# Optimization experiments

Hardware: AMD Instinct MI355X
Metric: run time of the kernel (lower is better)

The kernel has to match this reference:

```python
import jax, jax.numpy as jnp
import numpy as np

B, H, W = 8, 512, 512
KSIZE = 11   # HVS Gaussian kernel size
SIGMA = 2.0
EPS = 1e-8


def _gauss_kernel():
    ax = jnp.arange(KSIZE, dtype=jnp.float32) - (KSIZE - 1) / 2.0
    g = jnp.exp(-(ax ** 2) / (2.0 * SIGMA ** 2))
    k = jnp.outer(g, g)
    return k / jnp.sum(k)


def _conv_same(x, k):
    # x: (B,1,H,W), k: (kh,kw) symmetric -> conv == correlation
    return jax.lax.conv_general_dilated(
        x, k[None, None, :, :], window_strides=(1, 1), padding='SAME',
        dimension_numbers=('NCHW', 'OIHW', 'NCHW'))


def setup_inputs() -> dict:
    key = jax.random.key(0)
    k1, k2, k3 = jax.random.split(key, 3)
    prob_map = jax.random.uniform(k1, (B, 1, H, W), dtype=jnp.float32,
                                  minval=0.01, maxval=0.99)
    c = jax.random.uniform(k2, (B, 1, H, W), dtype=jnp.float32)
    # binary halftone sampled per-pixel from prob_map
    h_sampled = (jax.random.uniform(k3, (B, 1, H, W)) < prob_map).astype(jnp.float32)
    return {"prob_map": prob_map, "c": c, "h_sampled": h_sampled}


def reference(prob_map, c, h_sampled):
    k = _gauss_kernel()
    # perceived error of the sampled halftone: e = G*h - c
    e = _conv_same(h_sampled, k) - c                     # (B,1,H,W)
    corr = _conv_same(e, k)                              # (G*e), G symmetric
    sum_k2 = jnp.sum(k * k)
    delta = 1.0 - 2.0 * h_sampled                        # flip change per pixel
    # reward_calc.compute_reward_with_flip, vectorized over all pixels:
    # E(flip at a) - E = 2*delta_a*(G*e)(a) + delta_a^2 * sum(G^2)
    reward = 2.0 * delta * corr + (delta ** 2) * sum_k2  # >0 means flip hurts
    log_prob = jnp.where(h_sampled > 0.5,
                         jnp.log(prob_map + EPS),
                         jnp.log(1.0 - prob_map + EPS))
    # local expected-gradient (REINFORCE) loss, averaged over batch
    loss = -jnp.sum(reward * log_prob) / prob_map.shape[0]
    return loss
```

## Files before the change

### kernel.cpp

```cpp
#include <hip/hip_runtime.h>

typedef float v2f __attribute__((ext_vector_type(2)));
typedef float v4f __attribute__((ext_vector_type(4)));

#define IMG 512
#define TS  32
#define NBLK 2048

#define A_STR  58
#define BT_STR 46
#define ET_STR 44
#define CT_STR 36

__device__ __forceinline__ v2f lo2(v4f v) { return __builtin_shufflevector(v, v, 0, 1); }
__device__ __forceinline__ v2f hi2(v4f v) { return __builtin_shufflevector(v, v, 2, 3); }

__device__ __forceinline__ v4f ldq(const float* __restrict__ hmap, size_t base,
                                   int x0, int y0, int idx) {
    int r = idx / 14, q = idx - r * 14;
    int gy = y0 - 10 + r, gx0 = x0 - 12 + 4 * q;
    v4f v = {0.f, 0.f, 0.f, 0.f};
    if ((unsigned)gy < IMG) {
        const float* hr = &hmap[base + ((size_t)gy << 9)];
        if (gx0 >= 0 && gx0 + 3 < IMG) {
            v = *(const v4f*)&hr[gx0];
        } else {
            if ((unsigned)(gx0 + 0) < IMG) v.x = hr[gx0 + 0];
            if ((unsigned)(gx0 + 1) < IMG) v.y = hr[gx0 + 1];
            if ((unsigned)(gx0 + 2) < IMG) v.z = hr[gx0 + 2];
            if ((unsigned)(gx0 + 3) < IMG) v.w = hr[gx0 + 3];
        }
    }
    return v;
}

__global__ __launch_bounds__(256, 6) void marl_fused(
    const float* __restrict__ prob,
    const float* __restrict__ cmap,
    const float* __restrict__ hmap,
    float* __restrict__ out)
{
    __shared__ __align__(16) float Abuf[52 * A_STR];
    __shared__ __align__(16) float Bbuf[56 * BT_STR];
    __shared__ float red[4];

    const float W[11] = {0.00881223f, 0.02714358f, 0.06511405f, 0.12164908f,
                         0.17699840f, 0.20056540f, 0.17699840f, 0.12164908f,
                         0.06511405f, 0.02714358f, 0.00881223f};
    v2f wv[11];
#pragma unroll
    for (int i = 0; i < 11; ++i) wv[i] = (v2f){W[i], W[i]};
    float w2 = 0.f;
#pragma unroll
    for (int i = 0; i < 11; ++i) w2 += W[i] * W[i];
    const float sumk2 = w2 * w2;
    const v2f z = {0.f, 0.f};

    const int tid = threadIdx.x;
    const int i0 = tid, i1 = tid + 256, i2 = tid + 512;

    const int T  = blockIdx.x;
    const int b  = T >> 8, r8 = T & 255;
    const int x0 = (r8 & 15) * TS, y0 = (r8 >> 4) * TS;
    const size_t base = (size_t)b << 18;

    const int p1run = tid % 7, p1q = tid / 7;
    const int p2p = tid % 21, p2eq = tid / 21;
    const int p3oyq = tid & 3, p3ex = tid >> 2;
    const int oy0e = 2 * (tid & 15), ox0 = 2 * (tid >> 4);

    v2f hv[2], pv[2];
    float creg[2][4];
    {
        v4f ha = ldq(hmap, base, x0, y0, i0);
        v4f hb = ldq(hmap, base, x0, y0, i1);
        v4f hc = (tid < 216) ? ldq(hmap, base, x0, y0, i2) : (v4f){0.f,0.f,0.f,0.f};
        if (tid < 231) {
#pragma unroll
            for (int h = 0; h < 2; ++h) {
                int gy = y0 - 5 + 2 * p2p + h;
#pragma unroll
                for (int c = 0; c < 4; ++c) {
                    int gx = x0 - 5 + 4 * p2eq + c;
                    creg[h][c] = ((unsigned)gy < IMG && (unsigned)gx < IMG)
                        ? cmap[base + ((size_t)gy << 9) + gx] : 0.f;
                }
            }
        }
#pragma unroll
        for (int h = 0; h < 2; ++h) {
            size_t rowb = base + ((size_t)(y0 + oy0e + h) << 9) + (x0 + ox0);
            hv[h] = *(const v2f*)&hmap[rowb];
            pv[h] = *(const v2f*)&prob[rowb];
        }
        { int r = i0 / 14, q = i0 - r * 14; *(v4f*)&Abuf[r * A_STR + 4 * q] = ha; }
        { int r = i1 / 14, q = i1 - r * 14; *(v4f*)&Abuf[r * A_STR + 4 * q] = hb; }
        if (tid < 216) { int r = i2 / 14, q = i2 - r * 14; *(v4f*)&Abuf[r * A_STR + 4 * q] = hc; }
    }
    __syncthreads();

    if (tid < 98) {
        int by0 = 6 * p1run;
        v2f accLo[6] = {z, z, z, z, z, z}, accHi[6] = {z, z, z, z, z, z};
#pragma unroll
        for (int i = 0; i < 16; ++i) {
            v4f a = *(const v4f*)&Abuf[(by0 + i) * A_STR + 4 * p1q];
            v2f lo = lo2(a), hi = hi2(a);
#pragma unroll
            for (int r = 0; r < 6; ++r) {
                int j = i - r;
                if (j >= 0 && j < 11) { accLo[r] += wv[j] * lo; accHi[r] += wv[j] * hi; }
            }
        }
#pragma unroll
        for (int r = 0; r < 6; ++r) {
            int by = by0 + r;
            Bbuf[(4 * p1q + 0) * BT_STR + by] = accLo[r].x;
            Bbuf[(4 * p1q + 1) * BT_STR + by] = accLo[r].y;
            Bbuf[(4 * p1q + 2) * BT_STR + by] = accHi[r].x;
            Bbuf[(4 * p1q + 3) * BT_STR + by] = accHi[r].y;
        }
    }
    __syncthreads();

    if (tid < 231) {
        int ex0 = 4 * p2eq, ey0 = 2 * p2p;
        v2f acc[4] = {z, z, z, z};
#pragma unroll
        for (int i = 0; i < 14; ++i) {
            v2f bb = *(const v2f*)&Bbuf[(ex0 + 2 + i) * BT_STR + ey0];
#pragma unroll
            for (int c = 0; c < 4; ++c) {
                int j = i - c;
                if (j >= 0 && j < 11) acc[c] += wv[j] * bb;
            }
        }
#pragma unroll
        for (int c = 0; c < 4; ++c) {
            int ex = ex0 + c;
            if (ex < 42) {
                int gx = x0 - 5 + ex;
                bool xin = (unsigned)gx < IMG;
#pragma unroll
                for (int h = 0; h < 2; ++h) {
                    int gy = y0 - 5 + ey0 + h;
                    float v = 0.f;
                    if (xin && (unsigned)gy < IMG)
                        v = acc[c][h] - creg[h][c];
                    Abuf[ex * ET_STR + ey0 + h] = v;
                }
            }
        }
    }
    __syncthreads();

    if (tid < 168) {
        int oy0 = 8 * p3oyq;
        const float* src = &Abuf[p3ex * ET_STR + oy0];
        v4f w0 = *(const v4f*)&src[0];
        v4f w1 = *(const v4f*)&src[4];
        v4f w2_ = *(const v4f*)&src[8];
        v4f w3 = *(const v4f*)&src[12];
        v4f w4 = *(const v4f*)&src[16];
        float win[20];
        *(v4f*)&win[0] = w0; *(v4f*)&win[4] = w1; *(v4f*)&win[8] = w2_;
        *(v4f*)&win[12] = w3; *(v4f*)&win[16] = w4;
        float o[8];
#pragma unroll
        for (int k = 0; k < 8; ++k) {
            float acc = 0.f;
#pragma unroll
            for (int j = 0; j < 11; ++j) acc += W[j] * win[k + j];
            o[k] = acc;
        }
        *(v4f*)&Bbuf[p3ex * CT_STR + oy0]     = (v4f){o[0], o[1], o[2], o[3]};
        *(v4f*)&Bbuf[p3ex * CT_STR + oy0 + 4] = (v4f){o[4], o[5], o[6], o[7]};
    }
    __syncthreads();

    float partial = 0.f;
    {
        v2f acc[2] = {z, z};
#pragma unroll
        for (int i = 0; i < 12; ++i) {
            v2f ct = *(const v2f*)&Bbuf[(ox0 + i) * CT_STR + oy0e];
#pragma unroll
            for (int c = 0; c < 2; ++c) {
                int j = i - c;
                if (j >= 0 && j < 11) acc[c] += wv[j] * ct;
            }
        }
#pragma unroll
        for (int h = 0; h < 2; ++h) {
#pragma unroll
            for (int c = 0; c < 2; ++c) {
                float h_ = hv[h][c], p_ = pv[h][c];
                float logp = __logf(h_ > 0.5f ? p_ + 1e-8f : 1.f - p_ + 1e-8f);
                float delta = 1.f - 2.f * h_;
                partial += (2.f * delta * acc[c][h] + sumk2) * logp;
            }
        }
    }

#pragma unroll
    for (int off = 32; off > 0; off >>= 1)
        partial += __shfl_down(partial, off, 64);
    if ((tid & 63) == 0) red[tid >> 6] = partial;
    __syncthreads();
    if (tid == 0) {
        float s = red[0] + red[1] + red[2] + red[3];
        atomicAdd(out, s * -0.125f);
    }
}

extern "C" void kernel_launch(void* const* d_in, const int* in_sizes, int n_in,
                              void* d_out, int out_size, void* d_ws, size_t ws_size,
                              hipStream_t stream) {
    const float* prob = (const float*)d_in[0];
    const float* cmap = (const float*)d_in[1];
    const float* hmap = (const float*)d_in[2];
    float* out = (float*)d_out;

    hipMemsetAsync(out, 0, sizeof(float), stream);

    marl_fused<<<dim3(NBLK), dim3(256), 0, stream>>>(prob, cmap, hmap, out);
}
```

Before: 103.1 us.

## Widen tiles to 64x32 and replace atomic accumulation with a two-pass reduction

Output tiles grow from 32x32 to 64x32 pixels, which halves the block count and cuts the relative overhead of the 10-pixel halo on both separable convolution passes. Each thread in every stage now handles more outputs. The memset and per-block atomicAdd are replaced by per-block partial sums written to the workspace and reduced by a second single-block kernel, which also makes the sum deterministic. In exchange, shared memory per block and register pressure rise, occupancy drops to 4 blocks per SIMD, and the extra kernel launch adds some fixed latency.

```diff
diff --git a/kernel.cpp b/kernel.cpp
--- a/kernel.cpp
+++ b/kernel.cpp
@@ -4,10 +4,9 @@
 typedef float v4f __attribute__((ext_vector_type(4)));
 
 #define IMG 512
-#define TS  32
-#define NBLK 2048
-
-#define A_STR  58
+#define NBLK 1024
+
+#define A_STR  92
 #define BT_STR 46
 #define ET_STR 44
 #define CT_STR 36
@@ -17,7 +16,7 @@
 
 __device__ __forceinline__ v4f ldq(const float* __restrict__ hmap, size_t base,
                                    int x0, int y0, int idx) {
-    int r = idx / 14, q = idx - r * 14;
+    int r = idx / 22, q = idx - r * 22;
     int gy = y0 - 10 + r, gx0 = x0 - 12 + 4 * q;
     v4f v = {0.f, 0.f, 0.f, 0.f};
     if ((unsigned)gy < IMG) {
@@ -34,14 +33,14 @@
     return v;
 }
 
-__global__ __launch_bounds__(256, 6) void marl_fused(
+__global__ __launch_bounds__(256, 4) void marl_fused(
     const float* __restrict__ prob,
     const float* __restrict__ cmap,
     const float* __restrict__ hmap,
-    float* __restrict__ out)
+    float* __restrict__ ws)
 {
     __shared__ __align__(16) float Abuf[52 * A_STR];
-    __shared__ __align__(16) float Bbuf[56 * BT_STR];
+    __shared__ __align__(16) float Bbuf[88 * BT_STR];
     __shared__ float red[4];
 
     const float W[11] = {0.00881223f, 0.02714358f, 0.06511405f, 0.12164908f,
@@ -57,31 +56,31 @@
     const v2f z = {0.f, 0.f};
 
     const int tid = threadIdx.x;
-    const int i0 = tid, i1 = tid + 256, i2 = tid + 512;
-
     const int T  = blockIdx.x;
-    const int b  = T >> 8, r8 = T & 255;
-    const int x0 = (r8 & 15) * TS, y0 = (r8 >> 4) * TS;
+    const int b  = T >> 7, r7 = T & 127;
+    const int x0 = (r7 & 7) << 6, y0 = (r7 >> 3) << 5;
     const size_t base = (size_t)b << 18;
 
     const int p1run = tid % 7, p1q = tid / 7;
-    const int p2p = tid % 21, p2eq = tid / 21;
-    const int p3oyq = tid & 3, p3ex = tid >> 2;
-    const int oy0e = 2 * (tid & 15), ox0 = 2 * (tid >> 4);
-
-    v2f hv[2], pv[2];
-    float creg[2][4];
+    const int p2p = tid % 21, p2exo = tid / 21;
+    const int p3ex = tid >> 1, p3oy0 = (tid & 1) << 4;
+    const int ox0 = (tid >> 4) << 2, oy0e = (tid & 15) << 1;
+
+    float creg[2][8];
+    v4f hq[2], pq[2];
     {
-        v4f ha = ldq(hmap, base, x0, y0, i0);
-        v4f hb = ldq(hmap, base, x0, y0, i1);
-        v4f hc = (tid < 216) ? ldq(hmap, base, x0, y0, i2) : (v4f){0.f,0.f,0.f,0.f};
-        if (tid < 231) {
+        v4f s0 = ldq(hmap, base, x0, y0, tid);
+        v4f s1 = ldq(hmap, base, x0, y0, tid + 256);
+        v4f s2 = ldq(hmap, base, x0, y0, tid + 512);
+        v4f s3 = ldq(hmap, base, x0, y0, tid + 768);
+        v4f s4 = (tid < 120) ? ldq(hmap, base, x0, y0, tid + 1024) : (v4f){0.f,0.f,0.f,0.f};
+        if (tid < 210) {
 #pragma unroll
             for (int h = 0; h < 2; ++h) {
                 int gy = y0 - 5 + 2 * p2p + h;
 #pragma unroll
-                for (int c = 0; c < 4; ++c) {
-                    int gx = x0 - 5 + 4 * p2eq + c;
+                for (int c = 0; c < 8; ++c) {
+                    int gx = x0 - 5 + 8 * p2exo + c;
                     creg[h][c] = ((unsigned)gy < IMG && (unsigned)gx < IMG)
                         ? cmap[base + ((size_t)gy << 9) + gx] : 0.f;
                 }
@@ -90,16 +89,19 @@
 #pragma unroll
         for (int h = 0; h < 2; ++h) {
             size_t rowb = base + ((size_t)(y0 + oy0e + h) << 9) + (x0 + ox0);
-            hv[h] = *(const v2f*)&hmap[rowb];
-            pv[h] = *(const v2f*)&prob[rowb];
-        }
-        { int r = i0 / 14, q = i0 - r * 14; *(v4f*)&Abuf[r * A_STR + 4 * q] = ha; }
-        { int r = i1 / 14, q = i1 - r * 14; *(v4f*)&Abuf[r * A_STR + 4 * q] = hb; }
-        if (tid < 216) { int r = i2 / 14, q = i2 - r * 14; *(v4f*)&Abuf[r * A_STR + 4 * q] = hc; }
-    }
-    __syncthreads();
-
-    if (tid < 98) {
+            hq[h] = *(const v4f*)&hmap[rowb];
+            pq[h] = *(const v4f*)&prob[rowb];
+        }
+        { int i = tid;       int r = i / 22, q = i - r * 22; *(v4f*)&Abuf[r * A_STR + 4 * q] = s0; }
+        { int i = tid + 256; int r = i / 22, q = i - r * 22; *(v4f*)&Abuf[r * A_STR + 4 * q] = s1; }
+        { int i = tid + 512; int r = i / 22, q = i - r * 22; *(v4f*)&Abuf[r * A_STR + 4 * q] = s2; }
+        { int i = tid + 768; int r = i / 22, q = i - r * 22; *(v4f*)&Abuf[r * A_STR + 4 * q] = s3; }
+        if (tid < 120) { int i = tid + 1024; int r = i / 22, q = i - r * 22;
+                         *(v4f*)&Abuf[r * A_STR + 4 * q] = s4; }
+    }
+    __syncthreads();
+
+    if (tid < 154) {
         int by0 = 6 * p1run;
         v2f accLo[6] = {z, z, z, z, z, z}, accHi[6] = {z, z, z, z, z, z};
 #pragma unroll
@@ -123,78 +125,76 @@
     }
     __syncthreads();
 
-    if (tid < 231) {
-        int ex0 = 4 * p2eq, ey0 = 2 * p2p;
+    if (tid < 210) {
+        int ex0 = 8 * p2exo, ey0 = 2 * p2p;
+        v2f acc[8] = {z, z, z, z, z, z, z, z};
+#pragma unroll
+        for (int i = 0; i < 18; ++i) {
+            int cb = ex0 + 2 + i; cb = cb > 85 ? 85 : cb;
+            v2f bb = *(const v2f*)&Bbuf[cb * BT_STR + ey0];
+#pragma unroll
+            for (int c = 0; c < 8; ++c) {
+                int j = i - c;
+                if (j >= 0 && j < 11) acc[c] += wv[j] * bb;
+            }
+        }
+#pragma unroll
+        for (int c = 0; c < 8; ++c) {
+            int ex = ex0 + c;
+            if (ex < 74) {
+                int gx = x0 - 5 + ex;
+                bool xin = (unsigned)gx < IMG;
+                v2f ev;
+#pragma unroll
+                for (int h = 0; h < 2; ++h) {
+                    int gy = y0 - 5 + ey0 + h;
+                    ev[h] = (xin && (unsigned)gy < IMG) ? acc[c][h] - creg[h][c] : 0.f;
+                }
+                *(v2f*)&Abuf[ex * ET_STR + ey0] = ev;
+            }
+        }
+    }
+    __syncthreads();
+
+    if (tid < 148) {
+        const float* src = &Abuf[p3ex * ET_STR + p3oy0];
+        float win[26];
+#pragma unroll
+        for (int k = 0; k < 6; ++k)
+            *(v4f*)&win[4 * k] = *(const v4f*)&src[4 * k];
+        *(v2f*)&win[24] = *(const v2f*)&src[24];
+        float o[16];
+#pragma unroll
+        for (int k = 0; k < 16; ++k) {
+            float acc = 0.f;
+#pragma unroll
+            for (int j = 0; j < 11; ++j) acc += W[j] * win[k + j];
+            o[k] = acc;
+        }
+#pragma unroll
+        for (int k = 0; k < 4; ++k)
+            *(v4f*)&Bbuf[p3ex * CT_STR + p3oy0 + 4 * k] =
+                (v4f){o[4 * k], o[4 * k + 1], o[4 * k + 2], o[4 * k + 3]};
+    }
+    __syncthreads();
+
+    float partial = 0.f;
+    {
         v2f acc[4] = {z, z, z, z};
 #pragma unroll
         for (int i = 0; i < 14; ++i) {
-            v2f bb = *(const v2f*)&Bbuf[(ex0 + 2 + i) * BT_STR + ey0];
+            v2f ct = *(const v2f*)&Bbuf[(ox0 + i) * CT_STR + oy0e];
 #pragma unroll
             for (int c = 0; c < 4; ++c) {
                 int j = i - c;
-                if (j >= 0 && j < 11) acc[c] += wv[j] * bb;
-            }
-        }
-#pragma unroll
-        for (int c = 0; c < 4; ++c) {
-            int ex = ex0 + c;
-            if (ex < 42) {
-                int gx = x0 - 5 + ex;
-                bool xin = (unsigned)gx < IMG;
-#pragma unroll
-                for (int h = 0; h < 2; ++h) {
-                    int gy = y0 - 5 + ey0 + h;
-                    float v = 0.f;
-                    if (xin && (unsigned)gy < IMG)
-                        v = acc[c][h] - creg[h][c];
-                    Abuf[ex * ET_STR + ey0 + h] = v;
-                }
-            }
-        }
-    }
-    __syncthreads();
-
-    if (tid < 168) {
-        int oy0 = 8 * p3oyq;
-        const float* src = &Abuf[p3ex * ET_STR + oy0];
-        v4f w0 = *(const v4f*)&src[0];
-        v4f w1 = *(const v4f*)&src[4];
-        v4f w2_ = *(const v4f*)&src[8];
-        v4f w3 = *(const v4f*)&src[12];
-        v4f w4 = *(const v4f*)&src[16];
-        float win[20];
-        *(v4f*)&win[0] = w0; *(v4f*)&win[4] = w1; *(v4f*)&win[8] = w2_;
-        *(v4f*)&win[12] = w3; *(v4f*)&win[16] = w4;
-        float o[8];
-#pragma unroll
-        for (int k = 0; k < 8; ++k) {
-            float acc = 0.f;
-#pragma unroll
-            for (int j = 0; j < 11; ++j) acc += W[j] * win[k + j];
-            o[k] = acc;
-        }
-        *(v4f*)&Bbuf[p3ex * CT_STR + oy0]     = (v4f){o[0], o[1], o[2], o[3]};
-        *(v4f*)&Bbuf[p3ex * CT_STR + oy0 + 4] = (v4f){o[4], o[5], o[6], o[7]};
-    }
-    __syncthreads();
-
-    float partial = 0.f;
-    {
-        v2f acc[2] = {z, z};
-#pragma unroll
-        for (int i = 0; i < 12; ++i) {
-            v2f ct = *(const v2f*)&Bbuf[(ox0 + i) * CT_STR + oy0e];
-#pragma unroll
-            for (int c = 0; c < 2; ++c) {
-                int j = i - c;
                 if (j >= 0 && j < 11) acc[c] += wv[j] * ct;
             }
         }
 #pragma unroll
         for (int h = 0; h < 2; ++h) {
 #pragma unroll
-            for (int c = 0; c < 2; ++c) {
-                float h_ = hv[h][c], p_ = pv[h][c];
+            for (int c = 0; c < 4; ++c) {
+                float h_ = hq[h][c], p_ = pq[h][c];
                 float logp = __logf(h_ > 0.5f ? p_ + 1e-8f : 1.f - p_ + 1e-8f);
                 float delta = 1.f - 2.f * h_;
                 partial += (2.f * delta * acc[c][h] + sumk2) * logp;
@@ -207,10 +207,23 @@
         partial += __shfl_down(partial, off, 64);
     if ((tid & 63) == 0) red[tid >> 6] = partial;
     __syncthreads();
-    if (tid == 0) {
-        float s = red[0] + red[1] + red[2] + red[3];
-        atomicAdd(out, s * -0.125f);
-    }
+    if (tid == 0)
+        ws[blockIdx.x] = red[0] + red[1] + red[2] + red[3];
+}
+
+__global__ __launch_bounds__(256) void marl_reduce(const float* __restrict__ ws,
+                                                   float* __restrict__ out)
+{
+    __shared__ float red[4];
+    const int tid = threadIdx.x;
+    float s = ws[tid] + ws[tid + 256] + ws[tid + 512] + ws[tid + 768];
+#pragma unroll
+    for (int off = 32; off > 0; off >>= 1)
+        s += __shfl_down(s, off, 64);
+    if ((tid & 63) == 0) red[tid >> 6] = s;
+    __syncthreads();
+    if (tid == 0)
+        out[0] = -0.125f * (red[0] + red[1] + red[2] + red[3]);
 }
 
 extern "C" void kernel_launch(void* const* d_in, const int* in_sizes, int n_in,
@@ -220,8 +233,8 @@
     const float* cmap = (const float*)d_in[1];
     const float* hmap = (const float*)d_in[2];
     float* out = (float*)d_out;
-
-    hipMemsetAsync(out, 0, sizeof(float), stream);
-
-    marl_fused<<<dim3(NBLK), dim3(256), 0, stream>>>(prob, cmap, hmap, out);
-}
+    float* ws  = (float*)d_ws;
+
+    marl_fused<<<dim3(NBLK), dim3(256), 0, stream>>>(prob, cmap, hmap, ws);
+    marl_reduce<<<dim3(1), dim3(256), 0, stream>>>(ws, out);
+}
```

Measured after the change: 83.15 us. -19.3%, faster.
